# Kernel tuning notes

Measured on AMD Instinct MI355X. Metric: run time of the kernel, lower is better.

Reference implementation:

```python
import jax, jax.numpy as jnp
import numpy as np

N_NODES = 50000
N_EDGES = 1600000
N_GRAPHS = 512
HID = 64


def _mlp_params(key, din, dout, scale=0.1):
    k1, k2, k3 = jax.random.split(key, 3)
    return (
        jax.random.normal(k1, (din, HID), jnp.float32) * scale, jnp.zeros((HID,), jnp.float32),
        jax.random.normal(k2, (HID, HID), jnp.float32) * scale, jnp.zeros((HID,), jnp.float32),
        jax.random.normal(k3, (HID, dout), jnp.float32) * scale, jnp.zeros((dout,), jnp.float32),
    )


def _mlp(x, w1, b1, w2, b2, w3, b3, out_act=None):
    h = jax.nn.relu(x @ w1 + b1)
    h = jax.nn.relu(h @ w2 + b2)
    o = h @ w3 + b3
    return o if out_act is None else out_act(o)


def setup_inputs() -> dict:
    key = jax.random.key(0)
    ks = jax.random.split(key, 8)
    nf = jax.random.normal(ks[0], (N_NODES, 1), jnp.float32)
    ef = jax.random.normal(ks[1], (N_EDGES, 1), jnp.float32)
    src = jax.random.randint(ks[2], (N_EDGES,), 0, N_NODES)
    dst = jax.random.randint(ks[3], (N_EDGES,), 0, N_NODES)
    graph_id = jnp.sort(jax.random.randint(ks[4], (N_NODES,), 0, N_GRAPHS))
    e_w1, e_b1, e_w2, e_b2, e_w3, e_b3 = _mlp_params(ks[5], 3, 1)   # edge model: [src_nf, dst_nf, ef] -> msg
    n_w1, n_b1, n_w2, n_b2, n_w3, n_b3 = _mlp_params(ks[6], 2, 1)   # node model: [nf, agg] -> unf
    m_w1, m_b1, m_w2, m_b2, m_w3, m_b3 = _mlp_params(ks[7], 1, 1)   # node-wise MLP with Sigmoid out_act
    return dict(nf=nf, ef=ef, src=src, dst=dst, graph_id=graph_id,
                e_w1=e_w1, e_b1=e_b1, e_w2=e_w2, e_b2=e_b2, e_w3=e_w3, e_b3=e_b3,
                n_w1=n_w1, n_b1=n_b1, n_w2=n_w2, n_b2=n_b2, n_w3=n_w3, n_b3=n_b3,
                m_w1=m_w1, m_b1=m_b1, m_w2=m_w2, m_b2=m_b2, m_w3=m_w3, m_b3=m_b3)


def reference(nf, ef, src, dst, graph_id,
              e_w1, e_b1, e_w2, e_b2, e_w3, e_b3,
              n_w1, n_b1, n_w2, n_b2, n_w3, n_b3,
              m_w1, m_b1, m_w2, m_b2, m_w3, m_b3):
    # MPNN layer: message on edges, sum-aggregate to dst nodes, node update
    em_in = jnp.concatenate([nf[src], nf[dst], ef], axis=-1)          # [E, 3]
    msg = _mlp(em_in, e_w1, e_b1, e_w2, e_b2, e_w3, e_b3)             # [E, 1]
    agg = jax.ops.segment_sum(msg, dst, num_segments=N_NODES)        # [N, 1]
    unf = _mlp(jnp.concatenate([nf, agg], axis=-1),
               n_w1, n_b1, n_w2, n_b2, n_w3, n_b3)                    # [N, 1]
    # node-wise MLP with Sigmoid output activation
    node_out = _mlp(unf, m_w1, m_b1, m_w2, m_b2, m_w3, m_b3,
                    out_act=jax.nn.sigmoid)                           # [N, 1]
    # sum readout per graph, then final sigmoid
    rd = jax.ops.segment_sum(node_out, graph_id, num_segments=N_GRAPHS)  # [G, 1]
    return jax.nn.sigmoid(rd)
```

## Files before the change

kernel.cpp:

```cpp
#include <hip/hip_runtime.h>
#include <math.h>

#define HID 64
#define BKT_SHIFT 13
#define BKT_RANGE 8192
#define CCHUNK 32

typedef __attribute__((ext_vector_type(8))) short short8;
typedef __attribute__((ext_vector_type(4))) float f32x4;
typedef unsigned long long ull;

union FragU {
    uint4 q;
    short8 v;
    uint32_t u[4];
};

__device__ __forceinline__ uint32_t cvt_pk_bf16(float lo, float hi) {
    uint32_t r;
    asm("v_cvt_pk_bf16_f32 %0, %1, %2" : "=v"(r) : "v"(lo), "v"(hi));
    return r;
}
__device__ __forceinline__ float bf16lo_f(uint32_t u) { return __uint_as_float(u << 16); }
__device__ __forceinline__ float bf16hi_f(uint32_t u) { return __uint_as_float(u & 0xFFFF0000u); }
__device__ __forceinline__ unsigned short bf16_of(float v) {
    return (unsigned short)(cvt_pk_bf16(v, 0.f) & 0xFFFFu);
}

__global__ void prep_kernel(
    const float* __restrict__ w1,  const float* __restrict__ b1,  const float* __restrict__ w2,
    const float* __restrict__ nw1, const float* __restrict__ nb1, const float* __restrict__ nw2,
    const float* __restrict__ mw1, const float* __restrict__ mb1, const float* __restrict__ mw2,
    unsigned short* __restrict__ w1x,  unsigned short* __restrict__ w2T,
    unsigned short* __restrict__ nw1x, unsigned short* __restrict__ nw2T,
    unsigned short* __restrict__ mw1x, unsigned short* __restrict__ mw2T)
{
    int t = blockIdx.x * 256 + threadIdx.x;
    if (t < 4096) {
        int j = t >> 6, k = t & 63;
        w2T [t] = bf16_of(w2 [k * HID + j]);
        nw2T[t] = bf16_of(nw2[k * HID + j]);
        mw2T[t] = bf16_of(mw2[k * HID + j]);
    }
    if (t < 512) {
        int j = t >> 3, k = t & 7;
        float ve = k == 0 ? w1[j] : k == 1 ? w1[HID + j] : k == 2 ? w1[2 * HID + j] : k == 3 ? b1[j] : 0.f;
        float vn = k == 0 ? nw1[j] : k == 1 ? nw1[HID + j] : k == 2 ? nb1[j] : 0.f;
        float vm = k == 0 ? mw1[j] : k == 1 ? mb1[j] : 0.f;
        w1x [t] = bf16_of(ve);
        nw1x[t] = bf16_of(vn);
        mw1x[t] = bf16_of(vm);
    }
}

__global__ __launch_bounds__(256, 2) void edge_mfma3_kernel(
    const float* __restrict__ nf, const float* __restrict__ ef,
    const int* __restrict__ src, const int* __restrict__ dst,
    const unsigned short* __restrict__ w1x, const unsigned short* __restrict__ w2T,
    const float* __restrict__ b2, const float* __restrict__ w3, const float* __restrict__ b3,
    uint2* __restrict__ recs, ull* __restrict__ offs,
    float* __restrict__ aggFb, int E, int B, int nbatch, int mode)
{
    __shared__ uint2 tile[4][4][16][16];

    const int tid  = threadIdx.x;
    const int lane = tid & 63;
    const int wid  = tid >> 6;
    const int g    = lane >> 4;
    const int eL   = lane & 15;

    FragU af1[4];
#pragma unroll
    for (int t = 0; t < 4; ++t) {
        uint4 q = *(const uint4*)&w1x[(t * 16 + eL) * 8];
        af1[t].q = (g == 0) ? q : make_uint4(0, 0, 0, 0);
    }
    FragU af2[4][2];
#pragma unroll
    for (int t = 0; t < 4; ++t)
#pragma unroll
        for (int h = 0; h < 2; ++h)
            af2[t][h].q = *(const uint4*)&w2T[(t * 16 + eL) * 64 + h * 32 + g * 8];

    f32x4 b2v4[4];
    uint32_t w3p[8];
#pragma unroll
    for (int t = 0; t < 4; ++t) {
        int j = t * 16 + g * 4;
        b2v4[t] = *(const f32x4*)&b2[j];
        f32x4 wv = *(const f32x4*)&w3[j];
        w3p[2 * t]     = cvt_pk_bf16(wv[0], wv[1]);
        w3p[2 * t + 1] = cvt_pk_bf16(wv[2], wv[3]);
    }
    const float b3c = b3[0];

    int bi   = blockIdx.x;
    if (bi >= nbatch) return;
    int eidx = bi * 256 + tid;
    int ei   = eidx < E ? eidx : E - 1;
    int dcur = dst[ei];
    float a  = nf[src[ei]];
    float b  = nf[dcur];
    float c  = ef[ei];

    for (;;) {
        const int nbi   = bi + gridDim.x;
        const bool hn   = nbi < nbatch;
        const int neidx = hn ? nbi * 256 + tid : eidx;
        const int nei   = neidx < E ? neidx : E - 1;
        const int ns    = src[nei];
        const int nd    = dst[nei];
        const float ncf = ef[nei];

#pragma unroll
        for (int s = 0; s < 4; ++s) {
            float av = __shfl(a, s * 16 + eL);
            float bv = __shfl(b, s * 16 + eL);
            float cv = __shfl(c, s * 16 + eL);
            FragU bin;
            bin.u[0] = (g == 0) ? cvt_pk_bf16(av, bv) : 0u;
            bin.u[1] = (g == 0) ? cvt_pk_bf16(cv, 1.0f) : 0u;
            bin.u[2] = 0u; bin.u[3] = 0u;
#pragma unroll
            for (int t = 0; t < 4; ++t) {
                f32x4 h4 = __builtin_amdgcn_mfma_f32_16x16x32_bf16(
                    af1[t].v, bin.v, (f32x4){0.f, 0.f, 0.f, 0.f}, 0, 0, 0);
                uint32_t p0 = cvt_pk_bf16(fmaxf(h4[0], 0.f), fmaxf(h4[1], 0.f));
                uint32_t p1 = cvt_pk_bf16(fmaxf(h4[2], 0.f), fmaxf(h4[3], 0.f));
                tile[wid][s][eL][(4 * t + g) ^ ((eL & 7) << 1)] = make_uint2(p0, p1);
            }
        }

        const float na = nf[ns];
        const float nb = nf[nd];

        float mymsg = 0.f;
#pragma unroll
        for (int s = 0; s < 4; ++s) {
            const uint4* row = (const uint4*)&tile[wid][s][eL][0];
            FragU bf0, bf1;
            bf0.q = row[(g)     ^ (eL & 7)];
            bf1.q = row[(4 + g) ^ (eL & 7)];

            float p = 0.f;
#pragma unroll
            for (int t = 0; t < 4; ++t) {
                f32x4 ac = __builtin_amdgcn_mfma_f32_16x16x32_bf16(af2[t][0].v, bf0.v, b2v4[t], 0, 0, 0);
                ac = __builtin_amdgcn_mfma_f32_16x16x32_bf16(af2[t][1].v, bf1.v, ac, 0, 0, 0);
                p = fmaf(fmaxf(ac[0], 0.f), bf16lo_f(w3p[2 * t]),     p);
                p = fmaf(fmaxf(ac[1], 0.f), bf16hi_f(w3p[2 * t]),     p);
                p = fmaf(fmaxf(ac[2], 0.f), bf16lo_f(w3p[2 * t + 1]), p);
                p = fmaf(fmaxf(ac[3], 0.f), bf16hi_f(w3p[2 * t + 1]), p);
            }
            p += __shfl_xor(p, 16);
            p += __shfl_xor(p, 32);
            if (s == g) mymsg = p + b3c;
        }

        const bool valid = eidx < E;

        if (mode == 1) {
            if (valid) atomicAdd(&aggFb[dcur], mymsg);
        } else {
            const int bkt = dcur >> BKT_SHIFT;
            const ull lt = (1ull << lane) - 1;
            int myslot = 0;
            int off = 0;
            uint32_t pack_lo = 0, pack_hi = 0;
            for (int bb = 0; bb < B; ++bb) {
                if (bb < 4) pack_lo |= (uint32_t)off << (8 * bb);
                else        pack_hi |= (uint32_t)off << (8 * (bb - 4));
                ull m = __ballot(valid && bkt == bb);
                if (valid && bkt == bb) myslot = off + (int)__popcll(m & lt);
                off += (int)__popcll(m);
            }
            pack_hi |= (uint32_t)off << 24;

            const size_t wgl = (size_t)bi * 4 + wid;
            if (valid) recs[wgl * 64 + myslot] = make_uint2((uint32_t)dcur, __float_as_uint(mymsg));
            if (lane == 0) offs[wgl] = ((ull)pack_hi << 32) | (ull)pack_lo;
        }

        if (!hn) break;
        bi = nbi; eidx = neidx; ei = nei;
        a = na; b = nb; c = ncf; dcur = nd;
    }
}

__global__ __launch_bounds__(256) void bucket_accum_kernel(
    const uint2* __restrict__ recs, const ull* __restrict__ offs,
    float* __restrict__ partial, int NW, int B)
{
    __shared__ float acc[BKT_RANGE];

    const int b = blockIdx.x / CCHUNK;
    const int c = blockIdx.x % CCHUNK;

    for (int i = threadIdx.x; i < BKT_RANGE; i += 256) acc[i] = 0.f;
    __syncthreads();

    const int wpc = (NW + CCHUNK - 1) / CCHUNK;
    const int w0 = c * wpc;
    const int w1 = (w0 + wpc < NW) ? w0 + wpc : NW;
    const int nb = b + 1;
    const int base_node = b << BKT_SHIFT;

    for (int w = w0 + threadIdx.x; w < w1; w += 256) {
        ull ov = offs[w];
        uint32_t lo = (uint32_t)ov, hi = (uint32_t)(ov >> 32);
        int ob = (int)(((b  < 4) ? (lo >> (8 * b))  : (hi >> (8 * (b  - 4)))) & 0xFF);
        int oe = (int)(((nb < 4) ? (lo >> (8 * nb)) : (hi >> (8 * (nb - 4)))) & 0xFF);
        const uint2* rb = recs + (size_t)w * 64;
        for (int r = ob; r < oe; ++r) {
            uint2 rec = rb[r];
            atomicAdd(&acc[(int)rec.x - base_node], __uint_as_float(rec.y));
        }
    }
    __syncthreads();

    float* pb = partial + ((size_t)b * CCHUNK + c) * BKT_RANGE;
    for (int i = threadIdx.x; i < BKT_RANGE; i += 256) pb[i] = acc[i];
}

__global__ __launch_bounds__(256) void bucket_reduce_kernel(
    const float* __restrict__ partial, float* __restrict__ agg, int N)
{
    int n = blockIdx.x * 256 + threadIdx.x;
    if (n >= N) return;
    int b = n >> BKT_SHIFT, nl = n & (BKT_RANGE - 1);
    const float* p = partial + (size_t)b * CCHUNK * BKT_RANGE + nl;
    float s = 0.f;
#pragma unroll 8
    for (int c = 0; c < CCHUNK; ++c) s += p[(size_t)c * BKT_RANGE];
    agg[n] = s;
}

__global__ __launch_bounds__(256, 2) void node_mfma3_kernel(
    const float* __restrict__ nf, const float* __restrict__ agg,
    const int* __restrict__ gid,
    const unsigned short* __restrict__ nw1x, const unsigned short* __restrict__ nw2T,
    const float* __restrict__ nb2, const float* __restrict__ nw3, const float* __restrict__ nb3,
    const unsigned short* __restrict__ mw1x, const unsigned short* __restrict__ mw2T,
    const float* __restrict__ mb2, const float* __restrict__ mw3, const float* __restrict__ mb3,
    float* __restrict__ rd, int N)
{
    __shared__ uint2 tile[4][4][16][16];

    const int tid  = threadIdx.x;
    const int lane = tid & 63;
    const int wid  = tid >> 6;
    const int g    = lane >> 4;
    const int eL   = lane & 15;

    const int idx = blockIdx.x * 256 + tid;
    const int i   = idx < N ? idx : N - 1;
    const float x0 = nf[i];
    const float x1 = agg[i];
    const int   gg = gid[i];

    float myunf = 0.f, o = 0.f;

    {
        FragU af1[4], af2[4][2];
        f32x4 b2v4[4]; uint32_t w3p[8];
#pragma unroll
        for (int t = 0; t < 4; ++t) {
            uint4 q = *(const uint4*)&nw1x[(t * 16 + eL) * 8];
            af1[t].q = (g == 0) ? q : make_uint4(0, 0, 0, 0);
#pragma unroll
            for (int h = 0; h < 2; ++h)
                af2[t][h].q = *(const uint4*)&nw2T[(t * 16 + eL) * 64 + h * 32 + g * 8];
            int j = t * 16 + g * 4;
            b2v4[t] = *(const f32x4*)&nb2[j];
            f32x4 wv = *(const f32x4*)&nw3[j];
            w3p[2 * t]     = cvt_pk_bf16(wv[0], wv[1]);
            w3p[2 * t + 1] = cvt_pk_bf16(wv[2], wv[3]);
        }

#pragma unroll
        for (int s = 0; s < 4; ++s) {
            float av = __shfl(x0, s * 16 + eL);
            float bv = __shfl(x1, s * 16 + eL);
            FragU bin;
            bin.u[0] = (g == 0) ? cvt_pk_bf16(av, bv) : 0u;
            bin.u[1] = (g == 0) ? cvt_pk_bf16(1.0f, 0.f) : 0u;
            bin.u[2] = 0u; bin.u[3] = 0u;
#pragma unroll
            for (int t = 0; t < 4; ++t) {
                f32x4 h4 = __builtin_amdgcn_mfma_f32_16x16x32_bf16(
                    af1[t].v, bin.v, (f32x4){0.f, 0.f, 0.f, 0.f}, 0, 0, 0);
                uint32_t p0 = cvt_pk_bf16(fmaxf(h4[0], 0.f), fmaxf(h4[1], 0.f));
                uint32_t p1 = cvt_pk_bf16(fmaxf(h4[2], 0.f), fmaxf(h4[3], 0.f));
                tile[wid][s][eL][(4 * t + g) ^ ((eL & 7) << 1)] = make_uint2(p0, p1);
            }
        }
#pragma unroll
        for (int s = 0; s < 4; ++s) {
            const uint4* row = (const uint4*)&tile[wid][s][eL][0];
            FragU bf0, bf1;
            bf0.q = row[(g)     ^ (eL & 7)];
            bf1.q = row[(4 + g) ^ (eL & 7)];
            float p = 0.f;
#pragma unroll
            for (int t = 0; t < 4; ++t) {
                f32x4 ac = __builtin_amdgcn_mfma_f32_16x16x32_bf16(af2[t][0].v, bf0.v, b2v4[t], 0, 0, 0);
                ac = __builtin_amdgcn_mfma_f32_16x16x32_bf16(af2[t][1].v, bf1.v, ac, 0, 0, 0);
                p = fmaf(fmaxf(ac[0], 0.f), bf16lo_f(w3p[2 * t]),     p);
                p = fmaf(fmaxf(ac[1], 0.f), bf16hi_f(w3p[2 * t]),     p);
                p = fmaf(fmaxf(ac[2], 0.f), bf16lo_f(w3p[2 * t + 1]), p);
                p = fmaf(fmaxf(ac[3], 0.f), bf16hi_f(w3p[2 * t + 1]), p);
            }
            p += __shfl_xor(p, 16);
            p += __shfl_xor(p, 32);
            if (s == g) myunf = p + nb3[0];
        }
    }

    {
        FragU af1[4], af2[4][2];
        f32x4 b2v4[4]; uint32_t w3p[8];
#pragma unroll
        for (int t = 0; t < 4; ++t) {
            uint4 q = *(const uint4*)&mw1x[(t * 16 + eL) * 8];
            af1[t].q = (g == 0) ? q : make_uint4(0, 0, 0, 0);
#pragma unroll
            for (int h = 0; h < 2; ++h)
                af2[t][h].q = *(const uint4*)&mw2T[(t * 16 + eL) * 64 + h * 32 + g * 8];
            int j = t * 16 + g * 4;
            b2v4[t] = *(const f32x4*)&mb2[j];
            f32x4 wv = *(const f32x4*)&mw3[j];
            w3p[2 * t]     = cvt_pk_bf16(wv[0], wv[1]);
            w3p[2 * t + 1] = cvt_pk_bf16(wv[2], wv[3]);
        }

#pragma unroll
        for (int s = 0; s < 4; ++s) {
            float uv = __shfl(myunf, s * 16 + eL);
            FragU bin;
            bin.u[0] = (g == 0) ? cvt_pk_bf16(uv, 1.0f) : 0u;
            bin.u[1] = 0u; bin.u[2] = 0u; bin.u[3] = 0u;
#pragma unroll
            for (int t = 0; t < 4; ++t) {
                f32x4 h4 = __builtin_amdgcn_mfma_f32_16x16x32_bf16(
                    af1[t].v, bin.v, (f32x4){0.f, 0.f, 0.f, 0.f}, 0, 0, 0);
                uint32_t p0 = cvt_pk_bf16(fmaxf(h4[0], 0.f), fmaxf(h4[1], 0.f));
                uint32_t p1 = cvt_pk_bf16(fmaxf(h4[2], 0.f), fmaxf(h4[3], 0.f));
                tile[wid][s][eL][(4 * t + g) ^ ((eL & 7) << 1)] = make_uint2(p0, p1);
            }
        }
#pragma unroll
        for (int s = 0; s < 4; ++s) {
            const uint4* row = (const uint4*)&tile[wid][s][eL][0];
            FragU bf0, bf1;
            bf0.q = row[(g)     ^ (eL & 7)];
            bf1.q = row[(4 + g) ^ (eL & 7)];
            float p = 0.f;
#pragma unroll
            for (int t = 0; t < 4; ++t) {
                f32x4 ac = __builtin_amdgcn_mfma_f32_16x16x32_bf16(af2[t][0].v, bf0.v, b2v4[t], 0, 0, 0);
                ac = __builtin_amdgcn_mfma_f32_16x16x32_bf16(af2[t][1].v, bf1.v, ac, 0, 0, 0);
                p = fmaf(fmaxf(ac[0], 0.f), bf16lo_f(w3p[2 * t]),     p);
                p = fmaf(fmaxf(ac[1], 0.f), bf16hi_f(w3p[2 * t]),     p);
                p = fmaf(fmaxf(ac[2], 0.f), bf16lo_f(w3p[2 * t + 1]), p);
                p = fmaf(fmaxf(ac[3], 0.f), bf16hi_f(w3p[2 * t + 1]), p);
            }
            p += __shfl_xor(p, 16);
            p += __shfl_xor(p, 32);
            if (s == g) o = p + mb3[0];
        }
    }

    const float node_out = 1.0f / (1.0f + expf(-o));

    {
        const bool ok = idx < N;
        float v = ok ? node_out : 0.0f;
        int ggv = gg;
#pragma unroll
        for (int d = 1; d < 64; d <<= 1) {
            float vup = __shfl_up(v, d);
            int   gup = __shfl_up(ggv, d);
            if (lane >= d && gup == ggv) v += vup;
        }
        int gdn = __shfl_down(ggv, 1);
        bool tail = (lane == 63) || (gdn != ggv);
        if (tail)
            atomicAdd(&rd[ggv], v);
    }
}

__global__ void readout_kernel(const float* __restrict__ rd,
                               float* __restrict__ out, int G)
{
    int g = blockIdx.x * blockDim.x + threadIdx.x;
    if (g < G) out[g] = 1.0f / (1.0f + expf(-rd[g]));
}

extern "C" void kernel_launch(void* const* d_in, const int* in_sizes, int n_in,
                              void* d_out, int out_size, void* d_ws, size_t ws_size,
                              hipStream_t stream)
{
    const float* nf  = (const float*)d_in[0];
    const float* ef  = (const float*)d_in[1];
    const int*   src = (const int*)  d_in[2];
    const int*   dst = (const int*)  d_in[3];
    const int*   gid = (const int*)  d_in[4];

    const float* e_w1 = (const float*)d_in[5];
    const float* e_b1 = (const float*)d_in[6];
    const float* e_w2 = (const float*)d_in[7];
    const float* e_b2 = (const float*)d_in[8];
    const float* e_w3 = (const float*)d_in[9];
    const float* e_b3 = (const float*)d_in[10];

    const float* n_w1 = (const float*)d_in[11];
    const float* n_b1 = (const float*)d_in[12];
    const float* n_w2 = (const float*)d_in[13];
    const float* n_b2 = (const float*)d_in[14];
    const float* n_w3 = (const float*)d_in[15];
    const float* n_b3 = (const float*)d_in[16];

    const float* m_w1 = (const float*)d_in[17];
    const float* m_b1 = (const float*)d_in[18];
    const float* m_w2 = (const float*)d_in[19];
    const float* m_b2 = (const float*)d_in[20];
    const float* m_w3 = (const float*)d_in[21];
    const float* m_b3 = (const float*)d_in[22];

    const int N = in_sizes[0];
    const int E = in_sizes[2];
    const int G = out_size;

    const int nbatch = (E + 255) / 256;
    const int NW = (E + 63) / 64;
    const int B  = (N + BKT_RANGE - 1) / BKT_RANGE;

    size_t wts_b  = 32 * 1024;
    size_t recs_b = (size_t)NW * 64 * sizeof(uint2);
    size_t offs_b = (size_t)NW * sizeof(ull);
    size_t part_b = (size_t)B * CCHUNK * BKT_RANGE * sizeof(float);
    size_t need   = wts_b + recs_b + offs_b + part_b + ((size_t)N + G) * sizeof(float);
    bool bucketok = (B <= 8) && (need <= ws_size);

    char* wp = (char*)d_ws;
    unsigned short* w1x  = (unsigned short*)(wp);
    unsigned short* nw1x = (unsigned short*)(wp + 1024);
    unsigned short* mw1x = (unsigned short*)(wp + 2048);
    unsigned short* w2T  = (unsigned short*)(wp + 4096);
    unsigned short* nw2T = (unsigned short*)(wp + 4096 + 8192);
    unsigned short* mw2T = (unsigned short*)(wp + 4096 + 16384);

    float* out = (float*)d_out;

    prep_kernel<<<16, 256, 0, stream>>>(
        e_w1, e_b1, e_w2, n_w1, n_b1, n_w2, m_w1, m_b1, m_w2,
        w1x, w2T, nw1x, nw2T, mw1x, mw2T);

    int egrid = nbatch < 1024 ? nbatch : 1024;

    if (bucketok) {
        uint2* recs    = (uint2*)(wp + wts_b);
        ull*   offs    = (ull*)(wp + wts_b + recs_b);
        float* partial = (float*)(wp + wts_b + recs_b + offs_b);
        float* agg     = (float*)(wp + wts_b + recs_b + offs_b + part_b);
        float* rd      = agg + N;

        hipMemsetAsync(rd, 0, (size_t)G * sizeof(float), stream);

        edge_mfma3_kernel<<<egrid, 256, 0, stream>>>(
            nf, ef, src, dst, w1x, w2T, e_b2, e_w3, e_b3,
            recs, offs, nullptr, E, B, nbatch, 0);

        bucket_accum_kernel<<<B * CCHUNK, 256, 0, stream>>>(
            recs, offs, partial, NW, B);

        bucket_reduce_kernel<<<(N + 255) / 256, 256, 0, stream>>>(
            partial, agg, N);

        node_mfma3_kernel<<<(N + 255) / 256, 256, 0, stream>>>(
            nf, agg, gid,
            nw1x, nw2T, n_b2, n_w3, n_b3,
            mw1x, mw2T, m_b2, m_w3, m_b3,
            rd, N);

        readout_kernel<<<(G + 255) / 256, 256, 0, stream>>>(rd, out, G);
    } else {
        float* agg = (float*)(wp + wts_b);
        float* rd  = agg + N;

        hipMemsetAsync(agg, 0, ((size_t)N + G) * sizeof(float), stream);

        edge_mfma3_kernel<<<egrid, 256, 0, stream>>>(
            nf, ef, src, dst, w1x, w2T, e_b2, e_w3, e_b3,
            nullptr, nullptr, agg, E, B, nbatch, 1);

        node_mfma3_kernel<<<(N + 255) / 256, 256, 0, stream>>>(
            nf, agg, gid,
            nw1x, nw2T, n_b2, n_w3, n_b3,
            mw1x, mw2T, m_b2, m_w3, m_b3,
            rd, N);

        readout_kernel<<<(G + 255) / 256, 256, 0, stream>>>(rd, out, G);
    }
}
```

Baseline: 79.49 us.

## Halve edge kernel LDS tile and raise occupancy with two-phase layer compute

The edge kernel now processes its four 16-edge slices in two phases of two, so the shared-memory hidden tile shrinks by half. Launch bounds go from 2 to 6 blocks per SIMD and the persistent grid from 1024 to 1536 blocks, aiming for more waves in flight to hide gather latency. The layer-3 dot product is split into four independent partial sums to shorten the FMA dependency chain. The tighter launch bound may force register spills, and two phases mean more LDS write/read round trips.

```diff
diff --git a/kernel.cpp b/kernel.cpp
--- a/kernel.cpp
+++ b/kernel.cpp
@@ -53,7 +53,7 @@
     }
 }
 
-__global__ __launch_bounds__(256, 2) void edge_mfma3_kernel(
+__global__ __launch_bounds__(256, 6) void edge_mfma4_kernel(
     const float* __restrict__ nf, const float* __restrict__ ef,
     const int* __restrict__ src, const int* __restrict__ dst,
     const unsigned short* __restrict__ w1x, const unsigned short* __restrict__ w2T,
@@ -61,7 +61,7 @@
     uint2* __restrict__ recs, ull* __restrict__ offs,
     float* __restrict__ aggFb, int E, int B, int nbatch, int mode)
 {
-    __shared__ uint2 tile[4][4][16][16];
+    __shared__ uint2 tile[4][2][16][16];
 
     const int tid  = threadIdx.x;
     const int lane = tid & 63;
@@ -112,49 +112,82 @@
         const int nd    = dst[nei];
         const float ncf = ef[nei];
 
-#pragma unroll
-        for (int s = 0; s < 4; ++s) {
-            float av = __shfl(a, s * 16 + eL);
-            float bv = __shfl(b, s * 16 + eL);
-            float cv = __shfl(c, s * 16 + eL);
-            FragU bin;
-            bin.u[0] = (g == 0) ? cvt_pk_bf16(av, bv) : 0u;
-            bin.u[1] = (g == 0) ? cvt_pk_bf16(cv, 1.0f) : 0u;
-            bin.u[2] = 0u; bin.u[3] = 0u;
-#pragma unroll
-            for (int t = 0; t < 4; ++t) {
-                f32x4 h4 = __builtin_amdgcn_mfma_f32_16x16x32_bf16(
-                    af1[t].v, bin.v, (f32x4){0.f, 0.f, 0.f, 0.f}, 0, 0, 0);
-                uint32_t p0 = cvt_pk_bf16(fmaxf(h4[0], 0.f), fmaxf(h4[1], 0.f));
-                uint32_t p1 = cvt_pk_bf16(fmaxf(h4[2], 0.f), fmaxf(h4[3], 0.f));
-                tile[wid][s][eL][(4 * t + g) ^ ((eL & 7) << 1)] = make_uint2(p0, p1);
-            }
-        }
-
-        const float na = nf[ns];
-        const float nb = nf[nd];
-
+        float na = 0.f, nb = 0.f;
         float mymsg = 0.f;
-#pragma unroll
-        for (int s = 0; s < 4; ++s) {
-            const uint4* row = (const uint4*)&tile[wid][s][eL][0];
-            FragU bf0, bf1;
-            bf0.q = row[(g)     ^ (eL & 7)];
-            bf1.q = row[(4 + g) ^ (eL & 7)];
-
-            float p = 0.f;
-#pragma unroll
-            for (int t = 0; t < 4; ++t) {
-                f32x4 ac = __builtin_amdgcn_mfma_f32_16x16x32_bf16(af2[t][0].v, bf0.v, b2v4[t], 0, 0, 0);
-                ac = __builtin_amdgcn_mfma_f32_16x16x32_bf16(af2[t][1].v, bf1.v, ac, 0, 0, 0);
-                p = fmaf(fmaxf(ac[0], 0.f), bf16lo_f(w3p[2 * t]),     p);
-                p = fmaf(fmaxf(ac[1], 0.f), bf16hi_f(w3p[2 * t]),     p);
-                p = fmaf(fmaxf(ac[2], 0.f), bf16lo_f(w3p[2 * t + 1]), p);
-                p = fmaf(fmaxf(ac[3], 0.f), bf16hi_f(w3p[2 * t + 1]), p);
-            }
-            p += __shfl_xor(p, 16);
-            p += __shfl_xor(p, 32);
-            if (s == g) mymsg = p + b3c;
+
+#pragma unroll
+        for (int ph = 0; ph < 2; ++ph) {
+#pragma unroll
+            for (int ss = 0; ss < 2; ++ss) {
+                const int s = 2 * ph + ss;
+                float av = __shfl(a, s * 16 + eL);
+                float bv = __shfl(b, s * 16 + eL);
+                float cv = __shfl(c, s * 16 + eL);
+                FragU bin;
+                bin.u[0] = (g == 0) ? cvt_pk_bf16(av, bv) : 0u;
+                bin.u[1] = (g == 0) ? cvt_pk_bf16(cv, 1.0f) : 0u;
+                bin.u[2] = 0u; bin.u[3] = 0u;
+#pragma unroll
+                for (int t = 0; t < 4; ++t) {
+                    f32x4 h4 = __builtin_amdgcn_mfma_f32_16x16x32_bf16(
+                        af1[t].v, bin.v, (f32x4){0.f, 0.f, 0.f, 0.f}, 0, 0, 0);
+                    uint32_t p0 = cvt_pk_bf16(fmaxf(h4[0], 0.f), fmaxf(h4[1], 0.f));
+                    uint32_t p1 = cvt_pk_bf16(fmaxf(h4[2], 0.f), fmaxf(h4[3], 0.f));
+                    tile[wid][ss][eL][(4 * t + g) ^ ((eL & 7) << 1)] = make_uint2(p0, p1);
+                }
+            }
+
+            if (ph == 0) {
+                na = nf[ns];
+                nb = nf[nd];
+            }
+
+#pragma unroll
+            for (int ss = 0; ss < 2; ++ss) {
+                const int s = 2 * ph + ss;
+                const uint4* row = (const uint4*)&tile[wid][ss][eL][0];
+                FragU bf0, bf1;
+                bf0.q = row[(g)     ^ (eL & 7)];
+                bf1.q = row[(4 + g) ^ (eL & 7)];
+
+                float q0, q1, q2, q3;
+                {
+                    f32x4 ac = __builtin_amdgcn_mfma_f32_16x16x32_bf16(af2[0][0].v, bf0.v, b2v4[0], 0, 0, 0);
+                    ac = __builtin_amdgcn_mfma_f32_16x16x32_bf16(af2[0][1].v, bf1.v, ac, 0, 0, 0);
+                    q0 = fmaxf(ac[0], 0.f) * bf16lo_f(w3p[0]);
+                    q0 = fmaf(fmaxf(ac[1], 0.f), bf16hi_f(w3p[0]), q0);
+                    q0 = fmaf(fmaxf(ac[2], 0.f), bf16lo_f(w3p[1]), q0);
+                    q0 = fmaf(fmaxf(ac[3], 0.f), bf16hi_f(w3p[1]), q0);
+                }
+                {
+                    f32x4 ac = __builtin_amdgcn_mfma_f32_16x16x32_bf16(af2[1][0].v, bf0.v, b2v4[1], 0, 0, 0);
+                    ac = __builtin_amdgcn_mfma_f32_16x16x32_bf16(af2[1][1].v, bf1.v, ac, 0, 0, 0);
+                    q1 = fmaxf(ac[0], 0.f) * bf16lo_f(w3p[2]);
+                    q1 = fmaf(fmaxf(ac[1], 0.f), bf16hi_f(w3p[2]), q1);
+                    q1 = fmaf(fmaxf(ac[2], 0.f), bf16lo_f(w3p[3]), q1);
+                    q1 = fmaf(fmaxf(ac[3], 0.f), bf16hi_f(w3p[3]), q1);
+                }
+                {
+                    f32x4 ac = __builtin_amdgcn_mfma_f32_16x16x32_bf16(af2[2][0].v, bf0.v, b2v4[2], 0, 0, 0);
+                    ac = __builtin_amdgcn_mfma_f32_16x16x32_bf16(af2[2][1].v, bf1.v, ac, 0, 0, 0);
+                    q2 = fmaxf(ac[0], 0.f) * bf16lo_f(w3p[4]);
+                    q2 = fmaf(fmaxf(ac[1], 0.f), bf16hi_f(w3p[4]), q2);
+                    q2 = fmaf(fmaxf(ac[2], 0.f), bf16lo_f(w3p[5]), q2);
+                    q2 = fmaf(fmaxf(ac[3], 0.f), bf16hi_f(w3p[5]), q2);
+                }
+                {
+                    f32x4 ac = __builtin_amdgcn_mfma_f32_16x16x32_bf16(af2[3][0].v, bf0.v, b2v4[3], 0, 0, 0);
+                    ac = __builtin_amdgcn_mfma_f32_16x16x32_bf16(af2[3][1].v, bf1.v, ac, 0, 0, 0);
+                    q3 = fmaxf(ac[0], 0.f) * bf16lo_f(w3p[6]);
+                    q3 = fmaf(fmaxf(ac[1], 0.f), bf16hi_f(w3p[6]), q3);
+                    q3 = fmaf(fmaxf(ac[2], 0.f), bf16lo_f(w3p[7]), q3);
+                    q3 = fmaf(fmaxf(ac[3], 0.f), bf16hi_f(w3p[7]), q3);
+                }
+                float p = (q0 + q1) + (q2 + q3);
+                p += __shfl_xor(p, 16);
+                p += __shfl_xor(p, 32);
+                if (s == g) mymsg = p + b3c;
+            }
         }
 
         const bool valid = eidx < E;
@@ -456,7 +489,7 @@
         e_w1, e_b1, e_w2, n_w1, n_b1, n_w2, m_w1, m_b1, m_w2,
         w1x, w2T, nw1x, nw2T, mw1x, mw2T);
 
-    int egrid = nbatch < 1024 ? nbatch : 1024;
+    int egrid = nbatch < 1536 ? nbatch : 1536;
 
     if (bucketok) {
         uint2* recs    = (uint2*)(wp + wts_b);
@@ -467,7 +500,7 @@
 
         hipMemsetAsync(rd, 0, (size_t)G * sizeof(float), stream);
 
-        edge_mfma3_kernel<<<egrid, 256, 0, stream>>>(
+        edge_mfma4_kernel<<<egrid, 256, 0, stream>>>(
             nf, ef, src, dst, w1x, w2T, e_b2, e_w3, e_b3,
             recs, offs, nullptr, E, B, nbatch, 0);
 
@@ -490,7 +523,7 @@
 
         hipMemsetAsync(agg, 0, ((size_t)N + G) * sizeof(float), stream);
 
-        edge_mfma3_kernel<<<egrid, 256, 0, stream>>>(
+        edge_mfma4_kernel<<<egrid, 256, 0, stream>>>(
             nf, ef, src, dst, w1x, w2T, e_b2, e_w3, e_b3,
             nullptr, nullptr, agg, E, B, nbatch, 1);
 
```

New measurement: 262.9 us. 3.31x slower.
